# Kernel tuning notes

Measured on AMD Instinct MI355X. Metric: run time of the kernel, lower is better.

Reference implementation:

```python
import jax, jax.numpy as jnp
import numpy as np

D = 128        # node/time feature dim (n_node_features)
E = 20         # edge feature dim (hard-coded in TGS)
N = 4096       # number of source nodes
K = 10         # neighbors per node (hard-coded n_neighbors=10)
NUM_NODES = 100000
NUM_EDGES = 500000


def setup_inputs() -> dict:
    key = jax.random.key(0)
    ks = jax.random.split(key, 11)
    node_features = jax.random.normal(ks[0], (NUM_NODES, D), jnp.float32)
    edge_features = jax.random.normal(ks[1], (NUM_EDGES, E), jnp.float32)
    source_nodes = jax.random.randint(ks[2], (N,), 0, NUM_NODES)
    timestamps = jax.random.uniform(ks[3], (N,), jnp.float32) * 1000.0
    neighbors1 = jax.random.randint(ks[4], (N, K), 0, NUM_NODES)
    edge_idxs1 = jax.random.randint(ks[5], (N, K), 0, NUM_EDGES)
    edge_times1 = jax.random.uniform(ks[6], (N, K), jnp.float32) * 1000.0
    neighbors2 = jax.random.randint(ks[7], (N * K, K), 0, NUM_NODES)
    edge_idxs2 = jax.random.randint(ks[8], (N * K, K), 0, NUM_EDGES)
    edge_times2 = jax.random.uniform(ks[9], (N * K, K), jnp.float32) * 1000.0
    # TimeEncode params (TGN init: w = 1/10^linspace(0,9,D), b = 0)
    time_w = jnp.asarray(1.0 / 10.0 ** np.linspace(0, 9, D), jnp.float32)
    time_b = jnp.zeros((D,), jnp.float32)
    pk = jax.random.split(ks[10], 4)
    s1 = float(1.0 / np.sqrt(2 * D + E))
    lin1_w = jax.random.uniform(pk[0], (2, 2 * D + E, D), jnp.float32, -s1, s1)
    lin1_b = jax.random.uniform(pk[1], (2, D), jnp.float32, -s1, s1)
    s2 = float(1.0 / np.sqrt(3 * D))
    lin2_w = jax.random.uniform(pk[2], (2, 3 * D, D), jnp.float32, -s2, s2)
    lin2_b = jax.random.uniform(pk[3], (2, D), jnp.float32, -s2, s2)
    return dict(node_features=node_features, edge_features=edge_features,
                source_nodes=source_nodes, timestamps=timestamps,
                neighbors1=neighbors1, edge_idxs1=edge_idxs1, edge_times1=edge_times1,
                neighbors2=neighbors2, edge_idxs2=edge_idxs2, edge_times2=edge_times2,
                time_w=time_w, time_b=time_b,
                lin1_w=lin1_w, lin1_b=lin1_b, lin2_w=lin2_w, lin2_b=lin2_b)


def reference(node_features, edge_features, source_nodes, timestamps,
              neighbors1, edge_idxs1, edge_times1,
              neighbors2, edge_idxs2, edge_times2,
              time_w, time_b, lin1_w, lin1_b, lin2_w, lin2_b):
    def time_enc(t):
        # TGN TimeEncode: cos(t * w + b), broadcast over feature dim
        return jnp.cos(t[..., None] * time_w + time_b)

    def aggregate(layer, src_feat, src_time_emb, nbr_emb, edge_time_emb, edge_feat):
        # GraphSumEmbedding.aggregate
        nf = jnp.concatenate([nbr_emb, edge_time_emb, edge_feat], axis=-1)  # [n, K, 2D+E]
        h = nf @ lin1_w[layer] + lin1_b[layer]                              # [n, K, D]
        nbr_sum = jax.nn.relu(h.sum(axis=1))                                # [n, D]
        sf = jnp.concatenate([src_feat, src_time_emb, nbr_sum], axis=-1)   # [n, 3D]
        return sf @ lin2_w[layer] + lin2_b[layer]                           # [n, D]

    n, k = neighbors1.shape
    ts1 = jnp.repeat(timestamps, k)  # timestamps for the N*K first-hop neighbors

    # recursion level 1 (layer index 0): embed the N*K first-hop neighbors;
    # their neighbors' (level-0) embeddings are raw node features.
    emb1 = aggregate(
        0,
        node_features[neighbors1.reshape(-1)],          # [N*K, D]
        time_enc(jnp.zeros_like(ts1)),                  # [N*K, D]
        node_features[neighbors2],                      # [N*K, K, D]
        time_enc(ts1[:, None] - edge_times2),           # [N*K, K, D]
        edge_features[edge_idxs2])                      # [N*K, K, E]

    # recursion level 2 (layer index 1): embed the N source nodes
    emb2 = aggregate(
        1,
        node_features[source_nodes],                    # [N, D]
        time_enc(jnp.zeros_like(timestamps)),           # [N, D]
        emb1.reshape(n, k, -1),                         # [N, K, D]
        time_enc(timestamps[:, None] - edge_times1),    # [N, K, D]
        edge_features[edge_idxs1])                      # [N, K, E]
    return emb2
```

## Files before the change

kernel.cpp:

```cpp
#include <hip/hip_runtime.h>

#define TGS_D 128
#define TGS_E 20
#define TGS_K 10
#define TGS_F1 276
#define LDA1 296
#define LDA2 264
#define RPB 16

typedef _Float16 f16;
typedef _Float16 f16x4 __attribute__((ext_vector_type(4)));
typedef _Float16 f16x8 __attribute__((ext_vector_type(8)));
typedef float    f32x4 __attribute__((ext_vector_type(4)));

__global__ void tgs_pack_w1(const float* __restrict__ W1, f16x8* __restrict__ PW1) {
    const int b = blockIdx.x, lane = threadIdx.x;
    const int layer = b / 72, rem = b % 72, ntile = rem / 9, kk = rem % 9;
    const int colg = ntile * 16 + (lane & 15);
    const int kbase = kk * 32 + (lane >> 4) * 8;
    f16x8 v;
    #pragma unroll
    for (int j = 0; j < 8; ++j) {
        const int k = kbase + j;
        v[j] = (k < TGS_F1) ? (f16)W1[(layer * TGS_F1 + k) * TGS_D + colg] : (f16)0.f;
    }
    PW1[b * 64 + lane] = v;
}

__global__ void tgs_pack_w2(const float* __restrict__ W2, f16x8* __restrict__ PW2) {
    const int b = blockIdx.x, lane = threadIdx.x;
    const int layer = b / 64, rem = b % 64, ntile = rem / 8, kk = rem % 8;
    const int colg = ntile * 16 + (lane & 15);
    const int kbase = kk * 32 + (lane >> 4) * 8;
    f16x8 v;
    #pragma unroll
    for (int j = 0; j < 8; ++j) {
        const int k = kbase + j;
        const int w2row = (k < TGS_D) ? k : (k + TGS_D);
        v[j] = (f16)W2[(layer * 3 * TGS_D + w2row) * TGS_D + colg];
    }
    PW2[b * 64 + lane] = v;
}

__global__ __launch_bounds__(128)
void tgs_tvec_kernel(const float* __restrict__ tb, const float* __restrict__ W2,
                     const float* __restrict__ B2, float* __restrict__ tvec) {
    const int l = blockIdx.x, d = threadIdx.x;
    const float* w = W2 + (l * 3 * TGS_D + TGS_D) * TGS_D;
    float acc = B2[l * TGS_D + d];
    for (int j = 0; j < TGS_D; ++j)
        acc = fmaf(__cosf(tb[j]), w[j * TGS_D + d], acc);
    tvec[l * TGS_D + d] = acc;
}

template<int LEVEL>
__global__ __launch_bounds__(256, 6)
void tgs_agg_kernel(
    const float* __restrict__ NF, const float* __restrict__ EF,
    const int* __restrict__ src_ids, const float* __restrict__ ts_arr,
    const int* __restrict__ nbr_idx,
    const int* __restrict__ eidx, const float* __restrict__ etime,
    const float* __restrict__ emb_in,
    const float* __restrict__ tw, const float* __restrict__ tb,
    const f16x8* __restrict__ PW1, const float* __restrict__ B1,
    const f16x8* __restrict__ PW2, const float* __restrict__ tvec,
    float* __restrict__ out)
{
    __shared__ f16 snf[RPB][LDA1];
    __shared__ f16 sf2[RPB][LDA2];
    __shared__ int   s_nbr[RPB * TGS_K];
    __shared__ int   s_eid[RPB * TGS_K];
    __shared__ float s_et [RPB * TGS_K];
    __shared__ float s_ts [RPB];

    const int tid = threadIdx.x;
    const int base_row = blockIdx.x * RPB;

    if (tid < RPB * TGS_K) {
        if (LEVEL == 1) s_nbr[tid] = nbr_idx[base_row * TGS_K + tid];
        s_eid[tid] = eidx[base_row * TGS_K + tid];
        s_et [tid] = etime[base_row * TGS_K + tid];
    }
    if (tid < RPB)
        s_ts[tid] = (LEVEL == 1) ? ts_arr[(base_row + tid) / TGS_K] : ts_arr[base_row + tid];
    __syncthreads();

    {
        const int sub = tid & 31;
        const int rr  = tid >> 5;
        const float4 wv = ((const float4*)tw)[sub];
        const float4 bv = ((const float4*)tb)[sub];
        #pragma unroll
        for (int h = 0; h < 2; ++h) {
            const int r   = h * 8 + rr;
            const int row = base_row + r;

            float4 a = make_float4(0.f, 0.f, 0.f, 0.f);
            if (LEVEL == 1) {
                #pragma unroll
                for (int k = 0; k < TGS_K; ++k) {
                    const int nb = s_nbr[r * TGS_K + k];
                    const float4 v = ((const float4*)(NF + nb * TGS_D))[sub];
                    a.x += v.x; a.y += v.y; a.z += v.z; a.w += v.w;
                }
            } else {
                #pragma unroll
                for (int k = 0; k < TGS_K; ++k) {
                    const float4 v = ((const float4*)(emb_in + (row * TGS_K + k) * TGS_D))[sub];
                    a.x += v.x; a.y += v.y; a.z += v.z; a.w += v.w;
                }
            }
            *(f16x4*)&snf[r][sub * 4] = f16x4{(f16)a.x, (f16)a.y, (f16)a.z, (f16)a.w};

            const int sid = src_ids[row];
            const float4 s = ((const float4*)(NF + sid * TGS_D))[sub];
            *(f16x4*)&sf2[r][sub * 4] = f16x4{(f16)s.x, (f16)s.y, (f16)s.z, (f16)s.w};

            const float ts = s_ts[r];
            float4 st = make_float4(0.f, 0.f, 0.f, 0.f);
            #pragma unroll
            for (int k = 0; k < TGS_K; ++k) {
                const float dt = ts - s_et[r * TGS_K + k];
                st.x += __cosf(fmaf(dt, wv.x, bv.x));
                st.y += __cosf(fmaf(dt, wv.y, bv.y));
                st.z += __cosf(fmaf(dt, wv.z, bv.z));
                st.w += __cosf(fmaf(dt, wv.w, bv.w));
            }
            *(f16x4*)&snf[r][TGS_D + sub * 4] = f16x4{(f16)st.x, (f16)st.y, (f16)st.z, (f16)st.w};

            if (sub < TGS_E / 4) {
                float4 e = make_float4(0.f, 0.f, 0.f, 0.f);
                #pragma unroll
                for (int k = 0; k < TGS_K; ++k) {
                    const int eb = s_eid[r * TGS_K + k];
                    const float4 v = ((const float4*)(EF + eb * TGS_E))[sub];
                    e.x += v.x; e.y += v.y; e.z += v.z; e.w += v.w;
                }
                *(f16x4*)&snf[r][2 * TGS_D + sub * 4] = f16x4{(f16)e.x, (f16)e.y, (f16)e.z, (f16)e.w};
            } else if (sub < 8) {
                *(f16x4*)&snf[r][2 * TGS_D + sub * 4] =
                    f16x4{(f16)0.f, (f16)0.f, (f16)0.f, (f16)0.f};
            }
        }
    }
    __syncthreads();

    const int lane = tid & 63;
    const int w    = tid >> 6;
    const int ccol = lane & 15;
    const int row0 = (lane >> 4) * 4;

    {
        f32x4 acc0 = {0.f, 0.f, 0.f, 0.f}, acc1 = acc0;
        const f16* abase = &snf[lane & 15][(lane >> 4) * 8];
        const int t0 = 2 * w, t1 = 2 * w + 1;
        #pragma unroll
        for (int kk = 0; kk < 9; ++kk) {
            const f16x8 af = *(const f16x8*)(abase + kk * 32);
            const f16x8 b0 = PW1[(t0 * 9 + kk) * 64 + lane];
            const f16x8 b1 = PW1[(t1 * 9 + kk) * 64 + lane];
            acc0 = __builtin_amdgcn_mfma_f32_16x16x32_f16(af, b0, acc0, 0, 0, 0);
            acc1 = __builtin_amdgcn_mfma_f32_16x16x32_f16(af, b1, acc1, 0, 0, 0);
        }
        const float b1v0 = 10.f * B1[t0 * 16 + ccol];
        const float b1v1 = 10.f * B1[t1 * 16 + ccol];
        #pragma unroll
        for (int i = 0; i < 4; ++i) {
            sf2[row0 + i][TGS_D + t0 * 16 + ccol] = (f16)fmaxf(acc0[i] + b1v0, 0.f);
            sf2[row0 + i][TGS_D + t1 * 16 + ccol] = (f16)fmaxf(acc1[i] + b1v1, 0.f);
        }
    }
    __syncthreads();

    {
        f32x4 acc0 = {0.f, 0.f, 0.f, 0.f}, acc1 = acc0;
        const f16* abase = &sf2[lane & 15][(lane >> 4) * 8];
        const int t0 = 2 * w, t1 = 2 * w + 1;
        #pragma unroll
        for (int kk = 0; kk < 8; ++kk) {
            const f16x8 af = *(const f16x8*)(abase + kk * 32);
            const f16x8 b0 = PW2[(t0 * 8 + kk) * 64 + lane];
            const f16x8 b1 = PW2[(t1 * 8 + kk) * 64 + lane];
            acc0 = __builtin_amdgcn_mfma_f32_16x16x32_f16(af, b0, acc0, 0, 0, 0);
            acc1 = __builtin_amdgcn_mfma_f32_16x16x32_f16(af, b1, acc1, 0, 0, 0);
        }
        const float tv0 = tvec[t0 * 16 + ccol];
        const float tv1 = tvec[t1 * 16 + ccol];
        #pragma unroll
        for (int i = 0; i < 4; ++i) {
            out[(base_row + row0 + i) * TGS_D + t0 * 16 + ccol] = acc0[i] + tv0;
            out[(base_row + row0 + i) * TGS_D + t1 * 16 + ccol] = acc1[i] + tv1;
        }
    }
}

extern "C" void kernel_launch(void* const* d_in, const int* in_sizes, int n_in,
                              void* d_out, int out_size, void* d_ws, size_t ws_size,
                              hipStream_t stream) {
    const float* NF   = (const float*)d_in[0];
    const float* EF   = (const float*)d_in[1];
    const int*   SRC  = (const int*)  d_in[2];
    const float* TS   = (const float*)d_in[3];
    const int*   NBR1 = (const int*)  d_in[4];
    const int*   EI1  = (const int*)  d_in[5];
    const float* ET1  = (const float*)d_in[6];
    const int*   NBR2 = (const int*)  d_in[7];
    const int*   EI2  = (const int*)  d_in[8];
    const float* ET2  = (const float*)d_in[9];
    const float* TW   = (const float*)d_in[10];
    const float* TB   = (const float*)d_in[11];
    const float* W1   = (const float*)d_in[12];
    const float* B1   = (const float*)d_in[13];
    const float* W2   = (const float*)d_in[14];
    const float* B2   = (const float*)d_in[15];

    float* emb1 = (float*)d_ws;
    char*  wsb  = (char*)d_ws + 40960 * TGS_D * 4;
    f16x8* PW1  = (f16x8*)wsb;
    f16x8* PW2  = (f16x8*)(wsb + 147456);
    float* tvec = (float*)(wsb + 147456 + 131072);

    tgs_pack_w1<<<2 * 8 * 9, 64, 0, stream>>>(W1, PW1);
    tgs_pack_w2<<<2 * 8 * 8, 64, 0, stream>>>(W2, PW2);
    tgs_tvec_kernel<<<2, 128, 0, stream>>>(TB, W2, B2, tvec);

    const int n1 = 4096 * TGS_K;
    const int n2 = 4096;

    tgs_agg_kernel<1><<<n1 / RPB, 256, 0, stream>>>(
        NF, EF, NBR1, TS, NBR2, EI2, ET2, nullptr,
        TW, TB, PW1, B1, PW2, tvec, emb1);

    tgs_agg_kernel<2><<<n2 / RPB, 256, 0, stream>>>(
        NF, EF, SRC, TS, nullptr, EI1, ET1, emb1,
        TW, TB,
        PW1 + 8 * 9 * 64, B1 + TGS_D,
        PW2 + 8 * 8 * 64, tvec + TGS_D,
        (float*)d_out);
}
```

Baseline: 74.30 us.

## Store level-1 embeddings in fp16, widen blocks to 512 threads, fuse setup kernels

Merges the three weight-pack and tvec kernels into one setup launch. The intermediate emb1 buffer is now stored as fp16, halving its write and read traffic. The aggregation kernel uses 512 threads, one row per 32-thread group and one 16-column MFMA tile per wave. Each wave preloads its B fragments into registers before the gather phase. This adds register pressure and costs some precision in the intermediate embeddings.

```diff
diff --git a/kernel.cpp b/kernel.cpp
--- a/kernel.cpp
+++ b/kernel.cpp
@@ -13,58 +13,62 @@
 typedef _Float16 f16x8 __attribute__((ext_vector_type(8)));
 typedef float    f32x4 __attribute__((ext_vector_type(4)));
 
-__global__ void tgs_pack_w1(const float* __restrict__ W1, f16x8* __restrict__ PW1) {
-    const int b = blockIdx.x, lane = threadIdx.x;
-    const int layer = b / 72, rem = b % 72, ntile = rem / 9, kk = rem % 9;
-    const int colg = ntile * 16 + (lane & 15);
-    const int kbase = kk * 32 + (lane >> 4) * 8;
-    f16x8 v;
-    #pragma unroll
-    for (int j = 0; j < 8; ++j) {
-        const int k = kbase + j;
-        v[j] = (k < TGS_F1) ? (f16)W1[(layer * TGS_F1 + k) * TGS_D + colg] : (f16)0.f;
-    }
-    PW1[b * 64 + lane] = v;
+__global__ __launch_bounds__(128)
+void tgs_setup(const float* __restrict__ W1, const float* __restrict__ W2,
+               const float* __restrict__ tb, const float* __restrict__ B2,
+               f16x8* __restrict__ PW1, f16x8* __restrict__ PW2,
+               float* __restrict__ tvec) {
+    const int b = blockIdx.x, tid = threadIdx.x;
+    if (b < 144) {
+        if (tid < 64) {
+            const int layer = b / 72, rem = b % 72, ntile = rem / 9, kk = rem % 9;
+            const int colg = ntile * 16 + (tid & 15);
+            const int kbase = kk * 32 + (tid >> 4) * 8;
+            f16x8 v;
+            #pragma unroll
+            for (int j = 0; j < 8; ++j) {
+                const int k = kbase + j;
+                v[j] = (k < TGS_F1) ? (f16)W1[(layer * TGS_F1 + k) * TGS_D + colg] : (f16)0.f;
+            }
+            PW1[b * 64 + tid] = v;
+        }
+    } else if (b < 272) {
+        if (tid < 64) {
+            const int bb = b - 144;
+            const int layer = bb / 64, rem = bb % 64, ntile = rem / 8, kk = rem % 8;
+            const int colg = ntile * 16 + (tid & 15);
+            const int kbase = kk * 32 + (tid >> 4) * 8;
+            f16x8 v;
+            #pragma unroll
+            for (int j = 0; j < 8; ++j) {
+                const int k = kbase + j;
+                const int w2row = (k < TGS_D) ? k : (k + TGS_D);
+                v[j] = (f16)W2[(layer * 3 * TGS_D + w2row) * TGS_D + colg];
+            }
+            PW2[bb * 64 + tid] = v;
+        }
+    } else {
+        const int l = b - 272, d = tid;
+        const float* w = W2 + (l * 3 * TGS_D + TGS_D) * TGS_D;
+        float acc = B2[l * TGS_D + d];
+        for (int j = 0; j < TGS_D; ++j)
+            acc = fmaf(__cosf(tb[j]), w[j * TGS_D + d], acc);
+        tvec[l * TGS_D + d] = acc;
+    }
 }
 
-__global__ void tgs_pack_w2(const float* __restrict__ W2, f16x8* __restrict__ PW2) {
-    const int b = blockIdx.x, lane = threadIdx.x;
-    const int layer = b / 64, rem = b % 64, ntile = rem / 8, kk = rem % 8;
-    const int colg = ntile * 16 + (lane & 15);
-    const int kbase = kk * 32 + (lane >> 4) * 8;
-    f16x8 v;
-    #pragma unroll
-    for (int j = 0; j < 8; ++j) {
-        const int k = kbase + j;
-        const int w2row = (k < TGS_D) ? k : (k + TGS_D);
-        v[j] = (f16)W2[(layer * 3 * TGS_D + w2row) * TGS_D + colg];
-    }
-    PW2[b * 64 + lane] = v;
-}
-
-__global__ __launch_bounds__(128)
-void tgs_tvec_kernel(const float* __restrict__ tb, const float* __restrict__ W2,
-                     const float* __restrict__ B2, float* __restrict__ tvec) {
-    const int l = blockIdx.x, d = threadIdx.x;
-    const float* w = W2 + (l * 3 * TGS_D + TGS_D) * TGS_D;
-    float acc = B2[l * TGS_D + d];
-    for (int j = 0; j < TGS_D; ++j)
-        acc = fmaf(__cosf(tb[j]), w[j * TGS_D + d], acc);
-    tvec[l * TGS_D + d] = acc;
-}
-
-template<int LEVEL>
-__global__ __launch_bounds__(256, 6)
+template<int LEVEL, typename OutT>
+__global__ __launch_bounds__(512, 4)
 void tgs_agg_kernel(
     const float* __restrict__ NF, const float* __restrict__ EF,
     const int* __restrict__ src_ids, const float* __restrict__ ts_arr,
     const int* __restrict__ nbr_idx,
     const int* __restrict__ eidx, const float* __restrict__ etime,
-    const float* __restrict__ emb_in,
+    const f16* __restrict__ emb_in,
     const float* __restrict__ tw, const float* __restrict__ tb,
     const f16x8* __restrict__ PW1, const float* __restrict__ B1,
     const f16x8* __restrict__ PW2, const float* __restrict__ tvec,
-    float* __restrict__ out)
+    OutT* __restrict__ out)
 {
     __shared__ f16 snf[RPB][LDA1];
     __shared__ f16 sf2[RPB][LDA2];
@@ -74,7 +78,14 @@
     __shared__ float s_ts [RPB];
 
     const int tid = threadIdx.x;
+    const int lane = tid & 63;
+    const int wid  = tid >> 6;
     const int base_row = blockIdx.x * RPB;
+
+    f16x8 bf1[9];
+    #pragma unroll
+    for (int kk = 0; kk < 9; ++kk)
+        bf1[kk] = PW1[(wid * 9 + kk) * 64 + lane];
 
     if (tid < RPB * TGS_K) {
         if (LEVEL == 1) s_nbr[tid] = nbr_idx[base_row * TGS_K + tid];
@@ -87,110 +98,95 @@
 
     {
         const int sub = tid & 31;
-        const int rr  = tid >> 5;
+        const int r   = tid >> 5;
+        const int row = base_row + r;
         const float4 wv = ((const float4*)tw)[sub];
         const float4 bv = ((const float4*)tb)[sub];
-        #pragma unroll
-        for (int h = 0; h < 2; ++h) {
-            const int r   = h * 8 + rr;
-            const int row = base_row + r;
-
-            float4 a = make_float4(0.f, 0.f, 0.f, 0.f);
-            if (LEVEL == 1) {
-                #pragma unroll
-                for (int k = 0; k < TGS_K; ++k) {
-                    const int nb = s_nbr[r * TGS_K + k];
-                    const float4 v = ((const float4*)(NF + nb * TGS_D))[sub];
-                    a.x += v.x; a.y += v.y; a.z += v.z; a.w += v.w;
-                }
-            } else {
-                #pragma unroll
-                for (int k = 0; k < TGS_K; ++k) {
-                    const float4 v = ((const float4*)(emb_in + (row * TGS_K + k) * TGS_D))[sub];
-                    a.x += v.x; a.y += v.y; a.z += v.z; a.w += v.w;
-                }
-            }
-            *(f16x4*)&snf[r][sub * 4] = f16x4{(f16)a.x, (f16)a.y, (f16)a.z, (f16)a.w};
-
-            const int sid = src_ids[row];
-            const float4 s = ((const float4*)(NF + sid * TGS_D))[sub];
-            *(f16x4*)&sf2[r][sub * 4] = f16x4{(f16)s.x, (f16)s.y, (f16)s.z, (f16)s.w};
-
-            const float ts = s_ts[r];
-            float4 st = make_float4(0.f, 0.f, 0.f, 0.f);
+
+        float4 a = make_float4(0.f, 0.f, 0.f, 0.f);
+        if (LEVEL == 1) {
             #pragma unroll
             for (int k = 0; k < TGS_K; ++k) {
-                const float dt = ts - s_et[r * TGS_K + k];
-                st.x += __cosf(fmaf(dt, wv.x, bv.x));
-                st.y += __cosf(fmaf(dt, wv.y, bv.y));
-                st.z += __cosf(fmaf(dt, wv.z, bv.z));
-                st.w += __cosf(fmaf(dt, wv.w, bv.w));
-            }
-            *(f16x4*)&snf[r][TGS_D + sub * 4] = f16x4{(f16)st.x, (f16)st.y, (f16)st.z, (f16)st.w};
-
-            if (sub < TGS_E / 4) {
-                float4 e = make_float4(0.f, 0.f, 0.f, 0.f);
-                #pragma unroll
-                for (int k = 0; k < TGS_K; ++k) {
-                    const int eb = s_eid[r * TGS_K + k];
-                    const float4 v = ((const float4*)(EF + eb * TGS_E))[sub];
-                    e.x += v.x; e.y += v.y; e.z += v.z; e.w += v.w;
-                }
-                *(f16x4*)&snf[r][2 * TGS_D + sub * 4] = f16x4{(f16)e.x, (f16)e.y, (f16)e.z, (f16)e.w};
-            } else if (sub < 8) {
-                *(f16x4*)&snf[r][2 * TGS_D + sub * 4] =
-                    f16x4{(f16)0.f, (f16)0.f, (f16)0.f, (f16)0.f};
-            }
+                const int nb = s_nbr[r * TGS_K + k];
+                const float4 v = ((const float4*)(NF + nb * TGS_D))[sub];
+                a.x += v.x; a.y += v.y; a.z += v.z; a.w += v.w;
+            }
+        } else {
+            #pragma unroll
+            for (int k = 0; k < TGS_K; ++k) {
+                const f16x4 v = ((const f16x4*)(emb_in + (row * TGS_K + k) * TGS_D))[sub];
+                a.x += (float)v[0]; a.y += (float)v[1]; a.z += (float)v[2]; a.w += (float)v[3];
+            }
+        }
+        *(f16x4*)&snf[r][sub * 4] = f16x4{(f16)a.x, (f16)a.y, (f16)a.z, (f16)a.w};
+
+        const int sid = src_ids[row];
+        const float4 s = ((const float4*)(NF + sid * TGS_D))[sub];
+        *(f16x4*)&sf2[r][sub * 4] = f16x4{(f16)s.x, (f16)s.y, (f16)s.z, (f16)s.w};
+
+        const float ts = s_ts[r];
+        float4 st = make_float4(0.f, 0.f, 0.f, 0.f);
+        #pragma unroll
+        for (int k = 0; k < TGS_K; ++k) {
+            const float dt = ts - s_et[r * TGS_K + k];
+            st.x += __cosf(fmaf(dt, wv.x, bv.x));
+            st.y += __cosf(fmaf(dt, wv.y, bv.y));
+            st.z += __cosf(fmaf(dt, wv.z, bv.z));
+            st.w += __cosf(fmaf(dt, wv.w, bv.w));
+        }
+        *(f16x4*)&snf[r][TGS_D + sub * 4] = f16x4{(f16)st.x, (f16)st.y, (f16)st.z, (f16)st.w};
+
+        if (sub < TGS_E / 4) {
+            float4 e = make_float4(0.f, 0.f, 0.f, 0.f);
+            #pragma unroll
+            for (int k = 0; k < TGS_K; ++k) {
+                const int eb = s_eid[r * TGS_K + k];
+                const float4 v = ((const float4*)(EF + eb * TGS_E))[sub];
+                e.x += v.x; e.y += v.y; e.z += v.z; e.w += v.w;
+            }
+            *(f16x4*)&snf[r][2 * TGS_D + sub * 4] = f16x4{(f16)e.x, (f16)e.y, (f16)e.z, (f16)e.w};
+        } else if (sub < 8) {
+            *(f16x4*)&snf[r][2 * TGS_D + sub * 4] =
+                f16x4{(f16)0.f, (f16)0.f, (f16)0.f, (f16)0.f};
         }
     }
     __syncthreads();
 
-    const int lane = tid & 63;
-    const int w    = tid >> 6;
     const int ccol = lane & 15;
     const int row0 = (lane >> 4) * 4;
 
+    f16x8 bf2[8];
     {
-        f32x4 acc0 = {0.f, 0.f, 0.f, 0.f}, acc1 = acc0;
-        const f16* abase = &snf[lane & 15][(lane >> 4) * 8];
-        const int t0 = 2 * w, t1 = 2 * w + 1;
+        f32x4 acc = {0.f, 0.f, 0.f, 0.f};
+        const f16* abase = &snf[ccol][(lane >> 4) * 8];
         #pragma unroll
         for (int kk = 0; kk < 9; ++kk) {
             const f16x8 af = *(const f16x8*)(abase + kk * 32);
-            const f16x8 b0 = PW1[(t0 * 9 + kk) * 64 + lane];
-            const f16x8 b1 = PW1[(t1 * 9 + kk) * 64 + lane];
-            acc0 = __builtin_amdgcn_mfma_f32_16x16x32_f16(af, b0, acc0, 0, 0, 0);
-            acc1 = __builtin_amdgcn_mfma_f32_16x16x32_f16(af, b1, acc1, 0, 0, 0);
-        }
-        const float b1v0 = 10.f * B1[t0 * 16 + ccol];
-        const float b1v1 = 10.f * B1[t1 * 16 + ccol];
-        #pragma unroll
-        for (int i = 0; i < 4; ++i) {
-            sf2[row0 + i][TGS_D + t0 * 16 + ccol] = (f16)fmaxf(acc0[i] + b1v0, 0.f);
-            sf2[row0 + i][TGS_D + t1 * 16 + ccol] = (f16)fmaxf(acc1[i] + b1v1, 0.f);
-        }
+            acc = __builtin_amdgcn_mfma_f32_16x16x32_f16(af, bf1[kk], acc, 0, 0, 0);
+        }
+        #pragma unroll
+        for (int kk = 0; kk < 8; ++kk)
+            bf2[kk] = PW2[(wid * 8 + kk) * 64 + lane];
+
+        const float b1v = 10.f * B1[wid * 16 + ccol];
+        #pragma unroll
+        for (int i = 0; i < 4; ++i)
+            sf2[row0 + i][TGS_D + wid * 16 + ccol] = (f16)fmaxf(acc[i] + b1v, 0.f);
     }
     __syncthreads();
 
     {
-        f32x4 acc0 = {0.f, 0.f, 0.f, 0.f}, acc1 = acc0;
-        const f16* abase = &sf2[lane & 15][(lane >> 4) * 8];
-        const int t0 = 2 * w, t1 = 2 * w + 1;
+        f32x4 acc = {0.f, 0.f, 0.f, 0.f};
+        const f16* abase = &sf2[ccol][(lane >> 4) * 8];
         #pragma unroll
         for (int kk = 0; kk < 8; ++kk) {
             const f16x8 af = *(const f16x8*)(abase + kk * 32);
-            const f16x8 b0 = PW2[(t0 * 8 + kk) * 64 + lane];
-            const f16x8 b1 = PW2[(t1 * 8 + kk) * 64 + lane];
-            acc0 = __builtin_amdgcn_mfma_f32_16x16x32_f16(af, b0, acc0, 0, 0, 0);
-            acc1 = __builtin_amdgcn_mfma_f32_16x16x32_f16(af, b1, acc1, 0, 0, 0);
-        }
-        const float tv0 = tvec[t0 * 16 + ccol];
-        const float tv1 = tvec[t1 * 16 + ccol];
-        #pragma unroll
-        for (int i = 0; i < 4; ++i) {
-            out[(base_row + row0 + i) * TGS_D + t0 * 16 + ccol] = acc0[i] + tv0;
-            out[(base_row + row0 + i) * TGS_D + t1 * 16 + ccol] = acc1[i] + tv1;
-        }
+            acc = __builtin_amdgcn_mfma_f32_16x16x32_f16(af, bf2[kk], acc, 0, 0, 0);
+        }
+        const float tv = tvec[wid * 16 + ccol];
+        #pragma unroll
+        for (int i = 0; i < 4; ++i)
+            out[(base_row + row0 + i) * TGS_D + wid * 16 + ccol] = (OutT)(acc[i] + tv);
     }
 }
 
@@ -214,24 +210,22 @@
     const float* W2   = (const float*)d_in[14];
     const float* B2   = (const float*)d_in[15];
 
-    float* emb1 = (float*)d_ws;
-    char*  wsb  = (char*)d_ws + 40960 * TGS_D * 4;
+    f16*   emb1 = (f16*)d_ws;
+    char*  wsb  = (char*)d_ws + 40960 * TGS_D * 2;
     f16x8* PW1  = (f16x8*)wsb;
     f16x8* PW2  = (f16x8*)(wsb + 147456);
     float* tvec = (float*)(wsb + 147456 + 131072);
 
-    tgs_pack_w1<<<2 * 8 * 9, 64, 0, stream>>>(W1, PW1);
-    tgs_pack_w2<<<2 * 8 * 8, 64, 0, stream>>>(W2, PW2);
-    tgs_tvec_kernel<<<2, 128, 0, stream>>>(TB, W2, B2, tvec);
+    tgs_setup<<<274, 128, 0, stream>>>(W1, W2, TB, B2, PW1, PW2, tvec);
 
     const int n1 = 4096 * TGS_K;
     const int n2 = 4096;
 
-    tgs_agg_kernel<1><<<n1 / RPB, 256, 0, stream>>>(
-        NF, EF, NBR1, TS, NBR2, EI2, ET2, nullptr,
+    tgs_agg_kernel<1, f16><<<n1 / RPB, 512, 0, stream>>>(
+        NF, EF, NBR1, TS, NBR2, EI2, ET2, (const f16*)nullptr,
         TW, TB, PW1, B1, PW2, tvec, emb1);
 
-    tgs_agg_kernel<2><<<n2 / RPB, 256, 0, stream>>>(
+    tgs_agg_kernel<2, float><<<n2 / RPB, 512, 0, stream>>>(
         NF, EF, SRC, TS, nullptr, EI1, ET1, emb1,
         TW, TB,
         PW1 + 8 * 9 * 64, B1 + TGS_D,
```

Result: slower. 76.45 us (+2.9%).
